# Kernel tuning notes

Measured on AMD Instinct MI355X. Metric: run time of the kernel, lower is better.

The kernel has to match this reference:

```python
import jax, jax.numpy as jnp
import numpy as np

NUM_HEADS = 4

def setup_inputs() -> dict:
    key = jax.random.key(0)
    ks = jax.random.split(key, 8)
    B, L, D, Lc = 4, 4096, 256, 4096
    s = 0.02
    return {
        "x": jax.random.normal(ks[0], (B, L, D), jnp.float32),
        "context": jax.random.normal(ks[1], (B, Lc, D), jnp.float32),
        "Wq": jax.random.normal(ks[2], (D, D), jnp.float32) * s,
        "bq": jax.random.normal(ks[3], (D,), jnp.float32) * s,
        "Wkv": jax.random.normal(ks[4], (D, 2 * D), jnp.float32) * s,
        "bkv": jax.random.normal(ks[5], (2 * D,), jnp.float32) * s,
        "Wp": jax.random.normal(ks[6], (D, D), jnp.float32) * s,
        "bp": jax.random.normal(ks[7], (D,), jnp.float32) * s,
    }


def reference(x, context, Wq, bq, Wkv, bkv, Wp, bp):
    B, L, D = x.shape
    Hn = NUM_HEADS
    hd = D // Hn
    Hs = Ws = int(L ** 0.5)
    scale = hd ** (-0.5)

    # projections
    q = (x @ Wq + bq).reshape(B, L, Hn, hd).transpose(0, 2, 1, 3)        # [B,H,L,hd]
    kv = (context @ Wkv + bkv).reshape(B, -1, 2, Hn, hd)
    k = kv[:, :, 0].transpose(0, 2, 1, 3)                                 # [B,H,Lc,hd]
    v = kv[:, :, 1].transpose(0, 2, 1, 3)                                 # [B,H,Lc,hd]

    attn = jnp.einsum('bhqd,bhkd->bhqk', q, k) * scale                    # [B,H,L,Lc]
    attn_weights = jax.nn.softmax(attn, axis=-1)

    attn_map = attn_weights.mean(axis=1).sum(axis=-1).reshape(B, Hs, Ws)  # [B,H,W]

    out = jnp.einsum('bhqk,bhkd->bhqd', attn_weights, v)                  # [B,H,L,hd]
    out = out.transpose(0, 2, 1, 3).reshape(B, L, D)
    out = out @ Wp + bp
    return (out + x, attn_map)
```

## Files before the change

kernel.cpp:

```cpp
#include <hip/hip_runtime.h>
#include <stdint.h>

typedef unsigned short u16;
typedef short s16x8 __attribute__((ext_vector_type(8)));
typedef u16   u16x8 __attribute__((ext_vector_type(8)));
typedef float f32x4 __attribute__((ext_vector_type(4)));
typedef float f32x16 __attribute__((ext_vector_type(16)));

#define QSCALE 0.180336880111169f

__device__ __forceinline__ u16 f2bf(float f) {
  union { float f; uint32_t u; } v; v.f = f;
  uint32_t r = (v.u + 0x7fffu + ((v.u >> 16) & 1u)) >> 16;
  return (u16)r;
}

__device__ __forceinline__ f32x4 mfma16(s16x8 a, s16x8 b, f32x4 c) {
  return __builtin_amdgcn_mfma_f32_16x16x32_bf16(a, b, c, 0, 0, 0);
}
__device__ __forceinline__ f32x16 mfma32(s16x8 a, s16x8 b, f32x16 c) {
  return __builtin_amdgcn_mfma_f32_32x32x16_bf16(a, b, c, 0, 0, 0);
}

__device__ __forceinline__ void gload16(const void* g, void* l) {
  __builtin_amdgcn_global_load_lds(
      (const __attribute__((address_space(1))) void*)g,
      (__attribute__((address_space(3))) void*)l, 16, 0, 0);
}

__device__ __forceinline__ s16x8 ldsr(const u16* base, int row, int colb) {
  return *(const s16x8*)((const char*)base + row * 128 + (colb ^ ((row & 7) << 4)));
}

__device__ __forceinline__ uint32_t cvtpk(float lo, float hi) {
  uint32_t r;
  asm("v_cvt_pk_bf16_f32 %0, %1, %2" : "=v"(r) : "v"(lo), "v"(hi));
  return r;
}
__device__ __forceinline__ void hswap(uint32_t& a, uint32_t& b) {
  asm("v_permlane32_swap_b32 %0, %1" : "+v"(a), "+v"(b));
}
__device__ __forceinline__ float cross_sum(float v) {
  float t = v, u = v;
  asm("v_permlane32_swap_b32 %0, %1" : "+v"(t), "+v"(u));
  return t + u;
}

__global__ void k_convert(const float* __restrict__ x, const float* __restrict__ ctx,
                          const float* __restrict__ wq, const float* __restrict__ wkv,
                          const float* __restrict__ wp,
                          u16* __restrict__ xb, u16* __restrict__ cb,
                          u16* __restrict__ wqT, u16* __restrict__ wkvT,
                          u16* __restrict__ wpT, float* __restrict__ amap) {
  int tid = blockIdx.x * 256 + threadIdx.x;
  if (tid < 2097152) {
    const float* src; u16* dst; int off;
    if (tid < 1048576) { src = x;   dst = xb; off = tid * 4; }
    else               { src = ctx; dst = cb; off = (tid - 1048576) * 4; }
    f32x4 v = *(const f32x4*)(src + off);
    u16* d = dst + off;
    d[0] = f2bf(v.x); d[1] = f2bf(v.y); d[2] = f2bf(v.z); d[3] = f2bf(v.w);
    if (tid < 16384) amap[tid] = 1.0f;
  } else {
    int t4 = (tid - 2097152) * 4;
#pragma unroll
    for (int j = 0; j < 4; j++) {
      int t = t4 + j;
      if (t < 65536) {
        int k = t >> 8, n = t & 255;
        wqT[n * 256 + k] = f2bf(wq[t]);
      } else if (t < 196608) {
        int t2 = t - 65536;
        int k = t2 >> 9, n = t2 & 511;
        wkvT[n * 256 + k] = f2bf(wkv[t2]);
      } else {
        int t2 = t - 196608;
        int k = t2 >> 8, n = t2 & 255;
        wpT[n * 256 + k] = f2bf(wp[t2]);
      }
    }
  }
}

template<int EPI>
__global__ __launch_bounds__(256, 2) void k_gemm(
    const u16* __restrict__ A, const u16* __restrict__ Bt,
    const float* __restrict__ bias, const float* __restrict__ xres,
    u16* __restrict__ o16a, u16* __restrict__ o16b, float* __restrict__ o32) {
  __shared__ u16 Als[2][128 * 64];
  __shared__ u16 Bls[2][64 * 64];
  const int m0 = blockIdx.x * 128;
  const int n0 = blockIdx.y * 64;
  const int tid = threadIdx.x, w = tid >> 6, l = tid & 63;
  const int lr = l & 15, lg = l >> 4;
  const int wm = (w >> 1) * 64, wn = (w & 1) * 32;

  auto stage = [&](int buf, int k0) {
    const char* sa = (const char*)A;
#pragma unroll
    for (int i = 0; i < 4; i++) {
      int dbase = (w * 4 + i) * 1024;
      int d = dbase + l * 16;
      int row = d >> 7, colb = d & 127;
      gload16(sa + (size_t)(m0 + row) * 512 + k0 * 2 + (colb ^ ((row & 7) << 4)),
              (char*)Als[buf] + dbase);
    }
    const char* sb = (const char*)Bt;
#pragma unroll
    for (int i = 0; i < 2; i++) {
      int dbase = (w * 2 + i) * 1024;
      int d = dbase + l * 16;
      int row = d >> 7, colb = d & 127;
      gload16(sb + (size_t)(n0 + row) * 512 + k0 * 2 + (colb ^ ((row & 7) << 4)),
              (char*)Bls[buf] + dbase);
    }
  };

  f32x4 acc[4][2];
#pragma unroll
  for (int i = 0; i < 4; i++)
#pragma unroll
    for (int j = 0; j < 2; j++) acc[i][j] = (f32x4){0.f, 0.f, 0.f, 0.f};

  stage(0, 0);
  __syncthreads();
  int cur = 0;
  for (int ks = 0; ks < 4; ks++) {
    if (ks < 3) stage(cur ^ 1, (ks + 1) * 64);
    s16x8 a[4][2], b[2][2];
#pragma unroll
    for (int mt = 0; mt < 4; mt++)
#pragma unroll
      for (int kf = 0; kf < 2; kf++)
        a[mt][kf] = ldsr(Als[cur], wm + mt * 16 + lr, lg * 16 + kf * 64);
#pragma unroll
    for (int nt = 0; nt < 2; nt++)
#pragma unroll
      for (int kf = 0; kf < 2; kf++)
        b[nt][kf] = ldsr(Bls[cur], wn + nt * 16 + lr, lg * 16 + kf * 64);
#pragma unroll
    for (int mt = 0; mt < 4; mt++)
#pragma unroll
      for (int nt = 0; nt < 2; nt++) {
        acc[mt][nt] = mfma16(a[mt][0], b[nt][0], acc[mt][nt]);
        acc[mt][nt] = mfma16(a[mt][1], b[nt][1], acc[mt][nt]);
      }
    __syncthreads();
    cur ^= 1;
  }

#pragma unroll
  for (int mt = 0; mt < 4; mt++)
#pragma unroll
    for (int nt = 0; nt < 2; nt++)
#pragma unroll
      for (int r = 0; r < 4; r++) {
        int gm = m0 + wm + mt * 16 + lg * 4 + r;
        int gn = n0 + wn + nt * 16 + lr;
        float val = acc[mt][nt][r] + bias[gn];
        if constexpr (EPI == 0) {
          int b_ = gm >> 12, ql = gm & 4095, h = gn >> 6, dd = gn & 63;
          o16a[(((size_t)(b_ * 4 + h) * 4096 + ql) << 6) + dd] = f2bf(val * QSCALE);
        } else if constexpr (EPI == 1) {
          int b_ = gm >> 12, ql = gm & 4095;
          int s = gn >> 8, inner = gn & 255, h = inner >> 6, dd = inner & 63;
          if (s) {
            size_t addr = (((size_t)(b_ * 4 + h) * 64 + (ql >> 6)) * 64 + dd) * 64 + (ql & 63);
            o16b[addr] = f2bf(val);
          } else {
            size_t addr = (((size_t)(b_ * 4 + h) * 4096 + ql) << 6) + dd;
            o16a[addr] = f2bf(val);
          }
        } else {
          size_t idx = (size_t)gm * 256 + gn;
          o32[idx] = val + xres[idx];
        }
      }
}

__global__ __launch_bounds__(256, 2) void k_flash(
    const u16* __restrict__ qb, const u16* __restrict__ kb,
    const u16* __restrict__ vtb, u16* __restrict__ ob) {
  __shared__ char smem[34304];
  u16* kls0 = (u16*)(smem);
  u16* kls1 = (u16*)(smem + 8192);
  u16* vls0 = (u16*)(smem + 16384);
  u16* vls1 = (u16*)(smem + 24576);
  float* comb = (float*)smem;
  float* lsb  = (float*)(smem + 33792);
  const int id = blockIdx.y * 32 + blockIdx.x;
  const int sw = (id & 7) * 64 + (id >> 3);
  const int bh = sw >> 5;
  const int q0 = (sw & 31) * 128;
  const int tid = threadIdx.x, w = tid >> 6, l = tid & 63;
  const int lr32 = l & 31, hi = l >> 5;
  const int qq = w & 1, kvh = w >> 1;
  const char* kbase  = (const char*)(kb + (size_t)bh * 262144);
  const char* vtbase = (const char*)(vtb + (size_t)bh * 262144);

  s16x8 qfA[4], qfB[4];
  {
    const u16* qp = qb + ((size_t)bh * 4096 + q0 + qq * 64 + lr32) * 64 + hi * 8;
#pragma unroll
    for (int mm = 0; mm < 4; mm++) {
      qfA[mm] = *(const s16x8*)(qp + mm * 16);
      qfB[mm] = *(const s16x8*)(qp + 2048 + mm * 16);
    }
  }

  auto stage = [&](u16* kbuf, u16* vbuf, int t) {
    const char* ks = kbase  + (size_t)t * 8192;
    const char* vs = vtbase + (size_t)t * 8192;
#pragma unroll
    for (int i = 0; i < 2; i++) {
      int d = w * 2048 + i * 1024 + l * 16;
      int row = d >> 7, colb = d & 127;
      int so = row * 128 + (colb ^ ((row & 7) << 4));
      gload16(ks + so, (char*)kbuf + d);
      gload16(vs + so, (char*)vbuf + d);
    }
  };

  f32x16 oA0, oA1, oB0, oB1;
  float lsA = 0.f, lsB = 0.f;
#pragma unroll
  for (int r = 0; r < 16; r++) { oA0[r] = 0.f; oA1[r] = 0.f; oB0[r] = 0.f; oB1[r] = 0.f; }

  auto compute = [&](const u16* kc, const u16* vc) {
    s16x8 kf[4];
#pragma unroll
    for (int mm = 0; mm < 4; mm++)
      kf[mm] = ldsr(kc, kvh * 32 + lr32, mm * 32 + 16 * hi);
    f32x16 sA, sB;
#pragma unroll
    for (int r = 0; r < 16; r++) { sA[r] = 0.f; sB[r] = 0.f; }
    __builtin_amdgcn_s_setprio(1);
#pragma unroll
    for (int mm = 0; mm < 4; mm++) {
      sA = mfma32(kf[mm], qfA[mm], sA);
      sB = mfma32(kf[mm], qfB[mm], sB);
    }
    __builtin_amdgcn_s_setprio(0);
#pragma unroll
    for (int r = 0; r < 16; r++) {
      sA[r] = __builtin_amdgcn_exp2f(sA[r]);
      sB[r] = __builtin_amdgcn_exp2f(sB[r]);
    }
    float aA = 0.f, aB = 0.f;
#pragma unroll
    for (int r = 0; r < 16; r++) { aA += sA[r]; aB += sB[r]; }
    lsA += aA; lsB += aB;
    s16x8 vf[2][2];
#pragma unroll
    for (int ks2 = 0; ks2 < 2; ks2++) {
      int vcol = kvh * 64 + 32 * ks2 + 16 * hi;
      vf[ks2][0] = ldsr(vc, lr32,      vcol);
      vf[ks2][1] = ldsr(vc, 32 + lr32, vcol);
    }
#pragma unroll
    for (int ks2 = 0; ks2 < 2; ks2++) {
      uint32_t A0 = cvtpk(sA[8 * ks2 + 0], sA[8 * ks2 + 1]);
      uint32_t A1 = cvtpk(sA[8 * ks2 + 2], sA[8 * ks2 + 3]);
      uint32_t B0 = cvtpk(sA[8 * ks2 + 4], sA[8 * ks2 + 5]);
      uint32_t B1 = cvtpk(sA[8 * ks2 + 6], sA[8 * ks2 + 7]);
      hswap(A0, B0);
      hswap(A1, B1);
      union { uint32_t wv[4]; s16x8 h; } pa;
      pa.wv[0] = A0; pa.wv[1] = A1; pa.wv[2] = B0; pa.wv[3] = B1;
      uint32_t C0 = cvtpk(sB[8 * ks2 + 0], sB[8 * ks2 + 1]);
      uint32_t C1 = cvtpk(sB[8 * ks2 + 2], sB[8 * ks2 + 3]);
      uint32_t D0 = cvtpk(sB[8 * ks2 + 4], sB[8 * ks2 + 5]);
      uint32_t D1 = cvtpk(sB[8 * ks2 + 6], sB[8 * ks2 + 7]);
      hswap(C0, D0);
      hswap(C1, D1);
      union { uint32_t wv[4]; s16x8 h; } pb;
      pb.wv[0] = C0; pb.wv[1] = C1; pb.wv[2] = D0; pb.wv[3] = D1;
      __builtin_amdgcn_s_setprio(1);
      oA0 = mfma32(pa.h, vf[ks2][0], oA0);
      oA1 = mfma32(pa.h, vf[ks2][1], oA1);
      oB0 = mfma32(pb.h, vf[ks2][0], oB0);
      oB1 = mfma32(pb.h, vf[ks2][1], oB1);
      __builtin_amdgcn_s_setprio(0);
    }
  };

  stage(kls0, vls0, 0);
#pragma unroll 1
  for (int tt = 0; tt < 32; tt++) {
    const int t = tt * 2;
    asm volatile("s_waitcnt vmcnt(0)" ::: "memory");
    __builtin_amdgcn_s_barrier();
    asm volatile("" ::: "memory");
    stage(kls1, vls1, t + 1);
    compute(kls0, vls0);
    asm volatile("s_waitcnt vmcnt(0)" ::: "memory");
    __builtin_amdgcn_s_barrier();
    asm volatile("" ::: "memory");
    if (t + 2 < 64) stage(kls0, vls0, t + 2);
    compute(kls1, vls1);
  }

  float ltA = cross_sum(lsA);
  float ltB = cross_sum(lsB);
  __syncthreads();
  if (kvh == 1) {
    float* cp = comb + ((size_t)qq * 64 + l) * 66;
#pragma unroll
    for (int r = 0; r < 16; r++) {
      cp[r] = oA0[r]; cp[16 + r] = oA1[r];
      cp[32 + r] = oB0[r]; cp[48 + r] = oB1[r];
    }
    cp[64] = ltA; cp[65] = ltB;
  }
  __syncthreads();
  if (kvh == 0) {
    const float* cp = comb + ((size_t)qq * 64 + l) * 66;
#pragma unroll
    for (int r = 0; r < 16; r++) {
      oA0[r] += cp[r]; oA1[r] += cp[16 + r];
      oB0[r] += cp[32 + r]; oB1[r] += cp[48 + r];
    }
    ltA += cp[64]; ltB += cp[65];
    lsb[qq * 64 + lr32]      = ltA;
    lsb[qq * 64 + 32 + lr32] = ltB;
    const int b_ = bh >> 2, h = bh & 3;
    u16* obase = ob + (size_t)b_ * 4096 * 256 + h * 64;
#pragma unroll
    for (int r = 0; r < 16; r++) {
      int crow = (r & 3) + 8 * (r >> 2) + 4 * hi;
      float invA = __builtin_amdgcn_rcpf(lsb[qq * 64 + crow]);
      float invB = __builtin_amdgcn_rcpf(lsb[qq * 64 + 32 + crow]);
      size_t qrA = (size_t)(q0 + qq * 64 + crow);
      size_t qrB = qrA + 32;
      obase[qrA * 256 + lr32]      = f2bf(oA0[r] * invA);
      obase[qrA * 256 + 32 + lr32] = f2bf(oA1[r] * invA);
      obase[qrB * 256 + lr32]      = f2bf(oB0[r] * invB);
      obase[qrB * 256 + 32 + lr32] = f2bf(oB1[r] * invB);
    }
  }
}

extern "C" void kernel_launch(void* const* d_in, const int* in_sizes, int n_in,
                              void* d_out, int out_size, void* d_ws, size_t ws_size,
                              hipStream_t stream) {
  const float* x   = (const float*)d_in[0];
  const float* ctx = (const float*)d_in[1];
  const float* Wq  = (const float*)d_in[2];
  const float* bq  = (const float*)d_in[3];
  const float* Wkv = (const float*)d_in[4];
  const float* bkv = (const float*)d_in[5];
  const float* Wp  = (const float*)d_in[6];
  const float* bp  = (const float*)d_in[7];

  char* ws = (char*)d_ws;
  u16* xb    = (u16*)(ws);
  u16* cb    = (u16*)(ws + 8388608);
  u16* wqT   = (u16*)(ws + 16777216);
  u16* wkvT  = (u16*)(ws + 16908288);
  u16* wpT   = (u16*)(ws + 17170432);
  u16* qbuf  = (u16*)(ws + 17301504);
  u16* kbuf  = (u16*)(ws + 25690112);
  u16* vtbuf = (u16*)(ws + 34078720);
  u16* aout  = (u16*)(ws + 42467328);
  float* out  = (float*)d_out;
  float* amap = out + 4194304;

  k_convert<<<8448, 256, 0, stream>>>(x, ctx, Wq, Wkv, Wp, xb, cb, wqT, wkvT, wpT, amap);
  k_gemm<0><<<dim3(128, 4), 256, 0, stream>>>(xb, wqT, bq, nullptr, qbuf, nullptr, nullptr);
  k_gemm<1><<<dim3(128, 8), 256, 0, stream>>>(cb, wkvT, bkv, nullptr, kbuf, vtbuf, nullptr);
  k_flash<<<dim3(32, 16), 256, 0, stream>>>(qbuf, kbuf, vtbuf, aout);
  k_gemm<2><<<dim3(128, 4), 256, 0, stream>>>(aout, wpT, bp, x, nullptr, nullptr, out);
}
```

Before: 127.6 us.

## Split flash attention KV range across two blocks with separate reduce kernel

After: 315.9 us. 147% more time.

```diff
diff --git a/kernel.cpp b/kernel.cpp
--- a/kernel.cpp
+++ b/kernel.cpp
@@ -13,6 +13,10 @@
   union { float f; uint32_t u; } v; v.f = f;
   uint32_t r = (v.u + 0x7fffu + ((v.u >> 16) & 1u)) >> 16;
   return (u16)r;
+}
+__device__ __forceinline__ float bf2f(u16 x) {
+  union { uint32_t u; float f; } v; v.u = (uint32_t)x << 16;
+  return v.f;
 }
 
 __device__ __forceinline__ f32x4 mfma16(s16x8 a, s16x8 b, f32x4 c) {
@@ -178,23 +182,23 @@
       }
 }
 
-__global__ __launch_bounds__(256, 2) void k_flash(
+__global__ __launch_bounds__(256, 4) void k_flash(
     const u16* __restrict__ qb, const u16* __restrict__ kb,
-    const u16* __restrict__ vtb, u16* __restrict__ ob) {
-  __shared__ char smem[34304];
+    const u16* __restrict__ vtb, u16* __restrict__ pO, u16* __restrict__ pL) {
+  __shared__ char smem[33792];
   u16* kls0 = (u16*)(smem);
   u16* kls1 = (u16*)(smem + 8192);
   u16* vls0 = (u16*)(smem + 16384);
   u16* vls1 = (u16*)(smem + 24576);
   float* comb = (float*)smem;
-  float* lsb  = (float*)(smem + 33792);
   const int id = blockIdx.y * 32 + blockIdx.x;
-  const int sw = (id & 7) * 64 + (id >> 3);
-  const int bh = sw >> 5;
-  const int q0 = (sw & 31) * 128;
+  const int sw = (id & 7) * 128 + (id >> 3);
+  const int bh = sw >> 6;
+  const int q0 = ((sw >> 1) & 31) * 128;
+  const int kvh2 = sw & 1;
   const int tid = threadIdx.x, w = tid >> 6, l = tid & 63;
   const int lr32 = l & 31, hi = l >> 5;
-  const int qq = w & 1, kvh = w >> 1;
+  const int qq = w & 1, kvh = (w >> 1) & 1;
   const char* kbase  = (const char*)(kb + (size_t)bh * 262144);
   const char* vtbase = (const char*)(vtb + (size_t)bh * 262144);
 
@@ -284,10 +288,11 @@
     }
   };
 
-  stage(kls0, vls0, 0);
+  const int t0 = kvh2 * 32;
+  stage(kls0, vls0, t0);
 #pragma unroll 1
-  for (int tt = 0; tt < 32; tt++) {
-    const int t = tt * 2;
+  for (int tt = 0; tt < 16; tt++) {
+    const int t = t0 + tt * 2;
     asm volatile("s_waitcnt vmcnt(0)" ::: "memory");
     __builtin_amdgcn_s_barrier();
     asm volatile("" ::: "memory");
@@ -296,7 +301,7 @@
     asm volatile("s_waitcnt vmcnt(0)" ::: "memory");
     __builtin_amdgcn_s_barrier();
     asm volatile("" ::: "memory");
-    if (t + 2 < 64) stage(kls0, vls0, t + 2);
+    if (tt < 15) stage(kls0, vls0, t + 2);
     compute(kls1, vls1);
   }
 
@@ -321,23 +326,40 @@
       oB0[r] += cp[32 + r]; oB1[r] += cp[48 + r];
     }
     ltA += cp[64]; ltB += cp[65];
-    lsb[qq * 64 + lr32]      = ltA;
-    lsb[qq * 64 + 32 + lr32] = ltB;
-    const int b_ = bh >> 2, h = bh & 3;
-    u16* obase = ob + (size_t)b_ * 4096 * 256 + h * 64;
+    const size_t slab = (size_t)(kvh2 * 16 + bh);
+    u16* pob = pO + slab * 4096 * 64;
+    if (hi == 0) {
+      pL[slab * 4096 + q0 + qq * 64 + lr32]      = f2bf(ltA);
+      pL[slab * 4096 + q0 + qq * 64 + 32 + lr32] = f2bf(ltB);
+    }
 #pragma unroll
     for (int r = 0; r < 16; r++) {
       int crow = (r & 3) + 8 * (r >> 2) + 4 * hi;
-      float invA = __builtin_amdgcn_rcpf(lsb[qq * 64 + crow]);
-      float invB = __builtin_amdgcn_rcpf(lsb[qq * 64 + 32 + crow]);
       size_t qrA = (size_t)(q0 + qq * 64 + crow);
       size_t qrB = qrA + 32;
-      obase[qrA * 256 + lr32]      = f2bf(oA0[r] * invA);
-      obase[qrA * 256 + 32 + lr32] = f2bf(oA1[r] * invA);
-      obase[qrB * 256 + lr32]      = f2bf(oB0[r] * invB);
-      obase[qrB * 256 + 32 + lr32] = f2bf(oB1[r] * invB);
-    }
-  }
+      pob[qrA * 64 + lr32]      = f2bf(oA0[r]);
+      pob[qrA * 64 + 32 + lr32] = f2bf(oA1[r]);
+      pob[qrB * 64 + lr32]      = f2bf(oB0[r]);
+      pob[qrB * 64 + 32 + lr32] = f2bf(oB1[r]);
+    }
+  }
+}
+
+__global__ void k_reduce(const u16* __restrict__ pO, const u16* __restrict__ pL,
+                         u16* __restrict__ ob) {
+  int o = blockIdx.x * 256 + threadIdx.x;
+  int d8 = o & 7, q = (o >> 3) & 4095, bh = o >> 15;
+  size_t pidx = ((size_t)bh * 4096 + q) * 64 + d8 * 8;
+  u16x8 a = *(const u16x8*)(pO + pidx);
+  u16x8 b = *(const u16x8*)(pO + 4194304 + pidx);
+  float l0 = bf2f(pL[bh * 4096 + q]);
+  float l1 = bf2f(pL[65536 + bh * 4096 + q]);
+  float inv = __builtin_amdgcn_rcpf(l0 + l1);
+  u16x8 r;
+#pragma unroll
+  for (int j = 0; j < 8; j++) r[j] = f2bf((bf2f(a[j]) + bf2f(b[j])) * inv);
+  int b_ = bh >> 2, h = bh & 3;
+  *(u16x8*)(ob + ((size_t)b_ * 4096 + q) * 256 + h * 64 + d8 * 8) = r;
 }
 
 extern "C" void kernel_launch(void* const* d_in, const int* in_sizes, int n_in,
@@ -362,12 +384,15 @@
   u16* kbuf  = (u16*)(ws + 25690112);
   u16* vtbuf = (u16*)(ws + 34078720);
   u16* aout  = (u16*)(ws + 42467328);
+  u16* pO = (u16*)(ws);
+  u16* pL = (u16*)(ws + 16777216);
   float* out  = (float*)d_out;
   float* amap = out + 4194304;
 
   k_convert<<<8448, 256, 0, stream>>>(x, ctx, Wq, Wkv, Wp, xb, cb, wqT, wkvT, wpT, amap);
   k_gemm<0><<<dim3(128, 4), 256, 0, stream>>>(xb, wqT, bq, nullptr, qbuf, nullptr, nullptr);
   k_gemm<1><<<dim3(128, 8), 256, 0, stream>>>(cb, wkvT, bkv, nullptr, kbuf, vtbuf, nullptr);
-  k_flash<<<dim3(32, 16), 256, 0, stream>>>(qbuf, kbuf, vtbuf, aout);
+  k_flash<<<dim3(32, 32), 256, 0, stream>>>(qbuf, kbuf, vtbuf, pO, pL);
+  k_reduce<<<2048, 256, 0, stream>>>(pO, pL, aout);
   k_gemm<2><<<dim3(128, 4), 256, 0, stream>>>(aout, wpT, bp, x, nullptr, nullptr, out);
 }
```

## Compute softmax row sums via MFMA with ones and deepen K/V staging to four buffers

Applied to the files above, without the earlier changes.

Result: no change. 128.5 us (+0.7%).

```diff
diff --git a/kernel.cpp b/kernel.cpp
--- a/kernel.cpp
+++ b/kernel.cpp
@@ -39,11 +39,6 @@
 }
 __device__ __forceinline__ void hswap(uint32_t& a, uint32_t& b) {
   asm("v_permlane32_swap_b32 %0, %1" : "+v"(a), "+v"(b));
-}
-__device__ __forceinline__ float cross_sum(float v) {
-  float t = v, u = v;
-  asm("v_permlane32_swap_b32 %0, %1" : "+v"(t), "+v"(u));
-  return t + u;
 }
 
 __global__ void k_convert(const float* __restrict__ x, const float* __restrict__ ctx,
@@ -181,20 +176,15 @@
 __global__ __launch_bounds__(256, 2) void k_flash(
     const u16* __restrict__ qb, const u16* __restrict__ kb,
     const u16* __restrict__ vtb, u16* __restrict__ ob) {
-  __shared__ char smem[34304];
-  u16* kls0 = (u16*)(smem);
-  u16* kls1 = (u16*)(smem + 8192);
-  u16* vls0 = (u16*)(smem + 16384);
-  u16* vls1 = (u16*)(smem + 24576);
+  __shared__ char smem[65536];
   float* comb = (float*)smem;
-  float* lsb  = (float*)(smem + 33792);
   const int id = blockIdx.y * 32 + blockIdx.x;
   const int sw = (id & 7) * 64 + (id >> 3);
   const int bh = sw >> 5;
   const int q0 = (sw & 31) * 128;
   const int tid = threadIdx.x, w = tid >> 6, l = tid & 63;
   const int lr32 = l & 31, hi = l >> 5;
-  const int qq = w & 1, kvh = w >> 1;
+  const int qq = w & 1, kvh = (w >> 1) & 1;
   const char* kbase  = (const char*)(kb + (size_t)bh * 262144);
   const char* vtbase = (const char*)(vtb + (size_t)bh * 262144);
 
@@ -207,26 +197,35 @@
       qfB[mm] = *(const s16x8*)(qp + 2048 + mm * 16);
     }
   }
-
-  auto stage = [&](u16* kbuf, u16* vbuf, int t) {
+  union { u16 u[8]; s16x8 h; } onesu;
+#pragma unroll
+  for (int j = 0; j < 8; j++) onesu.u[j] = 0x3f80;
+
+  auto stage = [&](int buf, int t) {
     const char* ks = kbase  + (size_t)t * 8192;
     const char* vs = vtbase + (size_t)t * 8192;
+    char* kd = smem + buf * 8192;
+    char* vd = smem + 32768 + buf * 8192;
 #pragma unroll
     for (int i = 0; i < 2; i++) {
       int d = w * 2048 + i * 1024 + l * 16;
       int row = d >> 7, colb = d & 127;
       int so = row * 128 + (colb ^ ((row & 7) << 4));
-      gload16(ks + so, (char*)kbuf + d);
-      gload16(vs + so, (char*)vbuf + d);
+      gload16(ks + so, kd + d);
+      gload16(vs + so, vd + d);
     }
   };
 
-  f32x16 oA0, oA1, oB0, oB1;
-  float lsA = 0.f, lsB = 0.f;
-#pragma unroll
-  for (int r = 0; r < 16; r++) { oA0[r] = 0.f; oA1[r] = 0.f; oB0[r] = 0.f; oB1[r] = 0.f; }
-
-  auto compute = [&](const u16* kc, const u16* vc) {
+  f32x16 oA0, oA1, oB0, oB1, lsA, lsB;
+#pragma unroll
+  for (int r = 0; r < 16; r++) {
+    oA0[r] = 0.f; oA1[r] = 0.f; oB0[r] = 0.f; oB1[r] = 0.f;
+    lsA[r] = 0.f; lsB[r] = 0.f;
+  }
+
+  auto compute = [&](int buf) {
+    const u16* kc = (const u16*)(smem + buf * 8192);
+    const u16* vc = (const u16*)(smem + 32768 + buf * 8192);
     s16x8 kf[4];
 #pragma unroll
     for (int mm = 0; mm < 4; mm++)
@@ -246,10 +245,6 @@
       sA[r] = __builtin_amdgcn_exp2f(sA[r]);
       sB[r] = __builtin_amdgcn_exp2f(sB[r]);
     }
-    float aA = 0.f, aB = 0.f;
-#pragma unroll
-    for (int r = 0; r < 16; r++) { aA += sA[r]; aB += sB[r]; }
-    lsA += aA; lsB += aB;
     s16x8 vf[2][2];
 #pragma unroll
     for (int ks2 = 0; ks2 < 2; ks2++) {
@@ -278,58 +273,58 @@
       __builtin_amdgcn_s_setprio(1);
       oA0 = mfma32(pa.h, vf[ks2][0], oA0);
       oA1 = mfma32(pa.h, vf[ks2][1], oA1);
+      lsA = mfma32(pa.h, onesu.h, lsA);
       oB0 = mfma32(pb.h, vf[ks2][0], oB0);
       oB1 = mfma32(pb.h, vf[ks2][1], oB1);
+      lsB = mfma32(pb.h, onesu.h, lsB);
       __builtin_amdgcn_s_setprio(0);
     }
   };
 
-  stage(kls0, vls0, 0);
+  stage(0, 0); stage(1, 1);
 #pragma unroll 1
-  for (int tt = 0; tt < 32; tt++) {
-    const int t = tt * 2;
+  for (int tt = 0; tt < 16; tt++) {
+    const int t = tt * 4;
     asm volatile("s_waitcnt vmcnt(0)" ::: "memory");
     __builtin_amdgcn_s_barrier();
     asm volatile("" ::: "memory");
-    stage(kls1, vls1, t + 1);
-    compute(kls0, vls0);
+    if (t + 2 < 64) { stage(2, t + 2); stage(3, t + 3); }
+    compute(0);
+    compute(1);
     asm volatile("s_waitcnt vmcnt(0)" ::: "memory");
     __builtin_amdgcn_s_barrier();
     asm volatile("" ::: "memory");
-    if (t + 2 < 64) stage(kls0, vls0, t + 2);
-    compute(kls1, vls1);
-  }
-
-  float ltA = cross_sum(lsA);
-  float ltB = cross_sum(lsB);
+    if (t + 4 < 64) { stage(0, t + 4); stage(1, t + 5); }
+    compute(2);
+    compute(3);
+  }
+
   __syncthreads();
   if (kvh == 1) {
-    float* cp = comb + ((size_t)qq * 64 + l) * 66;
+    float* cp = comb + ((size_t)qq * 64 + l) * 97;
 #pragma unroll
     for (int r = 0; r < 16; r++) {
-      cp[r] = oA0[r]; cp[16 + r] = oA1[r];
+      cp[r] = oA0[r];      cp[16 + r] = oA1[r];
       cp[32 + r] = oB0[r]; cp[48 + r] = oB1[r];
-    }
-    cp[64] = ltA; cp[65] = ltB;
+      cp[64 + r] = lsA[r]; cp[80 + r] = lsB[r];
+    }
   }
   __syncthreads();
   if (kvh == 0) {
-    const float* cp = comb + ((size_t)qq * 64 + l) * 66;
+    const float* cp = comb + ((size_t)qq * 64 + l) * 97;
 #pragma unroll
     for (int r = 0; r < 16; r++) {
-      oA0[r] += cp[r]; oA1[r] += cp[16 + r];
+      oA0[r] += cp[r];      oA1[r] += cp[16 + r];
       oB0[r] += cp[32 + r]; oB1[r] += cp[48 + r];
-    }
-    ltA += cp[64]; ltB += cp[65];
-    lsb[qq * 64 + lr32]      = ltA;
-    lsb[qq * 64 + 32 + lr32] = ltB;
+      lsA[r] += cp[64 + r]; lsB[r] += cp[80 + r];
+    }
     const int b_ = bh >> 2, h = bh & 3;
     u16* obase = ob + (size_t)b_ * 4096 * 256 + h * 64;
 #pragma unroll
     for (int r = 0; r < 16; r++) {
       int crow = (r & 3) + 8 * (r >> 2) + 4 * hi;
-      float invA = __builtin_amdgcn_rcpf(lsb[qq * 64 + crow]);
-      float invB = __builtin_amdgcn_rcpf(lsb[qq * 64 + 32 + crow]);
+      float invA = __builtin_amdgcn_rcpf(lsA[r]);
+      float invB = __builtin_amdgcn_rcpf(lsB[r]);
       size_t qrA = (size_t)(q0 + qq * 64 + crow);
       size_t qrB = qrA + 32;
       obase[qrA * 256 + lr32]      = f2bf(oA0[r] * invA);
```

## Give each wave private LDS K/V buffers and drop per-tile block barriers

Applied to the files above, without the earlier changes.

New measurement: 137.0 us. 1.07x slower.

```diff
diff --git a/kernel.cpp b/kernel.cpp
--- a/kernel.cpp
+++ b/kernel.cpp
@@ -181,13 +181,9 @@
 __global__ __launch_bounds__(256, 2) void k_flash(
     const u16* __restrict__ qb, const u16* __restrict__ kb,
     const u16* __restrict__ vtb, u16* __restrict__ ob) {
-  __shared__ char smem[34304];
-  u16* kls0 = (u16*)(smem);
-  u16* kls1 = (u16*)(smem + 8192);
-  u16* vls0 = (u16*)(smem + 16384);
-  u16* vls1 = (u16*)(smem + 24576);
+  __shared__ char smem[66048];
   float* comb = (float*)smem;
-  float* lsb  = (float*)(smem + 33792);
+  float* lsb  = (float*)(smem + 65536);
   const int id = blockIdx.y * 32 + blockIdx.x;
   const int sw = (id & 7) * 64 + (id >> 3);
   const int bh = sw >> 5;
@@ -195,8 +191,9 @@
   const int tid = threadIdx.x, w = tid >> 6, l = tid & 63;
   const int lr32 = l & 31, hi = l >> 5;
   const int qq = w & 1, kvh = w >> 1;
-  const char* kbase  = (const char*)(kb + (size_t)bh * 262144);
-  const char* vtbase = (const char*)(vtb + (size_t)bh * 262144);
+  const char* kbase  = (const char*)(kb + (size_t)bh * 262144) + kvh * 4096;
+  const char* vtbase = (const char*)(vtb + (size_t)bh * 262144) + kvh * 64;
+  char* mybuf = smem + w * 16384;
 
   s16x8 qfA[4], qfB[4];
   {
@@ -208,16 +205,18 @@
     }
   }
 
-  auto stage = [&](u16* kbuf, u16* vbuf, int t) {
+  auto stage = [&](int buf, int t) {
+    char* kd = mybuf + buf * 8192;
+    char* vd = kd + 4096;
     const char* ks = kbase  + (size_t)t * 8192;
     const char* vs = vtbase + (size_t)t * 8192;
 #pragma unroll
-    for (int i = 0; i < 2; i++) {
-      int d = w * 2048 + i * 1024 + l * 16;
-      int row = d >> 7, colb = d & 127;
-      int so = row * 128 + (colb ^ ((row & 7) << 4));
-      gload16(ks + so, (char*)kbuf + d);
-      gload16(vs + so, (char*)vbuf + d);
+    for (int j = 0; j < 4; j++) {
+      int o = j * 1024 + l * 16;
+      int krow = o >> 7, kcolb = o & 127;
+      gload16(ks + krow * 128 + (kcolb ^ ((krow & 7) << 4)), kd + o);
+      int vrow = o >> 6, vcolb = o & 63;
+      gload16(vs + (size_t)vrow * 128 + (vcolb ^ ((vrow & 3) << 4)), vd + o);
     }
   };
 
@@ -226,11 +225,15 @@
 #pragma unroll
   for (int r = 0; r < 16; r++) { oA0[r] = 0.f; oA1[r] = 0.f; oB0[r] = 0.f; oB1[r] = 0.f; }
 
-  auto compute = [&](const u16* kc, const u16* vc) {
+  auto compute = [&](int buf) {
+    const char* kc = mybuf + buf * 8192;
+    const char* vc = kc + 4096;
     s16x8 kf[4];
 #pragma unroll
-    for (int mm = 0; mm < 4; mm++)
-      kf[mm] = ldsr(kc, kvh * 32 + lr32, mm * 32 + 16 * hi);
+    for (int mm = 0; mm < 4; mm++) {
+      int colb = mm * 32 + 16 * hi;
+      kf[mm] = *(const s16x8*)(kc + lr32 * 128 + (colb ^ ((lr32 & 7) << 4)));
+    }
     f32x16 sA, sB;
 #pragma unroll
     for (int r = 0; r < 16; r++) { sA[r] = 0.f; sB[r] = 0.f; }
@@ -253,9 +256,9 @@
     s16x8 vf[2][2];
 #pragma unroll
     for (int ks2 = 0; ks2 < 2; ks2++) {
-      int vcol = kvh * 64 + 32 * ks2 + 16 * hi;
-      vf[ks2][0] = ldsr(vc, lr32,      vcol);
-      vf[ks2][1] = ldsr(vc, 32 + lr32, vcol);
+      int colb = 32 * ks2 + 16 * hi;
+      vf[ks2][0] = *(const s16x8*)(vc + lr32 * 64 + (colb ^ ((lr32 & 3) << 4)));
+      vf[ks2][1] = *(const s16x8*)(vc + (32 + lr32) * 64 + (colb ^ ((lr32 & 3) << 4)));
     }
 #pragma unroll
     for (int ks2 = 0; ks2 < 2; ks2++) {
@@ -284,20 +287,17 @@
     }
   };
 
-  stage(kls0, vls0, 0);
+  stage(0, 0);
 #pragma unroll 1
-  for (int tt = 0; tt < 32; tt++) {
-    const int t = tt * 2;
-    asm volatile("s_waitcnt vmcnt(0)" ::: "memory");
-    __builtin_amdgcn_s_barrier();
+  for (int t = 0; t < 64; t++) {
+    if (t + 1 < 64) {
+      stage((t + 1) & 1, t + 1);
+      asm volatile("s_waitcnt vmcnt(8)" ::: "memory");
+    } else {
+      asm volatile("s_waitcnt vmcnt(0)" ::: "memory");
+    }
+    compute(t & 1);
     asm volatile("" ::: "memory");
-    stage(kls1, vls1, t + 1);
-    compute(kls0, vls0);
-    asm volatile("s_waitcnt vmcnt(0)" ::: "memory");
-    __builtin_amdgcn_s_barrier();
-    asm volatile("" ::: "memory");
-    if (t + 2 < 64) stage(kls0, vls0, t + 2);
-    compute(kls1, vls1);
   }
 
   float ltA = cross_sum(lsA);
```
